# Kernel optimization log

Measured on AMD Instinct MI355X. Metric: run time of the kernel, lower is better.

## Reference

```python
import jax, jax.numpy as jnp
import numpy as np

NUM_HEADS = 4

def _pos_encoding(seq_len, d, dtype):
    # standard sinusoidal positional encoding [seq_len, d]
    pos = jnp.arange(seq_len, dtype=jnp.float32)[:, None]
    i = jnp.arange(0, d, 2, dtype=jnp.float32)
    div = jnp.exp(-jnp.log(10000.0) * i / d)
    ang = pos * div
    pe = jnp.zeros((seq_len, d), jnp.float32)
    pe = pe.at[:, 0::2].set(jnp.sin(ang)).at[:, 1::2].set(jnp.cos(ang))
    return pe.astype(dtype)

def _layer_norm(x, g, b, eps=1e-5):
    m = jnp.mean(x, axis=-1, keepdims=True)
    v = jnp.mean(jnp.square(x - m), axis=-1, keepdims=True)
    return (x - m) / jnp.sqrt(v + eps) * g + b

def setup_inputs() -> dict:
    key = jax.random.key(0)
    ks = jax.random.split(key, 10)
    B, S, H, W, N = 8, 512, 768, 8, 4096
    s = 0.02
    token_reps = jax.random.normal(ks[0], (B, S, H), jnp.float32)
    starts = jax.random.randint(ks[1], (B, N), 0, S - W)
    widths = jax.random.randint(ks[2], (B, N), 1, W + 1)
    span_ids = jnp.stack([starts, starts + widths], axis=-1)  # end > start, end <= S
    span_masks = jax.random.randint(ks[3], (B, N), 0, 2)
    return dict(
        token_reps=token_reps,
        dummy_query=jax.random.normal(ks[4], (H,), jnp.float32) * s,
        in_proj_w=jax.random.normal(ks[5], (3 * H, H), jnp.float32) * s,
        in_proj_b=jnp.zeros((3 * H,), jnp.float32),
        out_w=jax.random.normal(ks[6], (H, H), jnp.float32) * s,
        out_b=jnp.zeros((H,), jnp.float32),
        ln_g=jnp.ones((H,), jnp.float32),
        ln_b=jnp.zeros((H,), jnp.float32),
        ffn_w1=jax.random.normal(ks[7], (H, 4 * H), jnp.float32) * s,
        ffn_b1=jnp.zeros((4 * H,), jnp.float32),
        ffn_w2=jax.random.normal(ks[8], (4 * H, H), jnp.float32) * s,
        ffn_b2=jnp.zeros((H,), jnp.float32),
        span_ids=span_ids,
        span_masks=span_masks,
    )

def reference(token_reps, dummy_query, in_proj_w, in_proj_b, out_w, out_b,
              ln_g, ln_b, ffn_w1, ffn_b1, ffn_w2, ffn_b2, span_ids, span_masks):
    B, S, H = token_reps.shape
    N = span_ids.shape[1]
    NH = NUM_HEADS
    DH = H // NH
    # sequence positional encoding (dropout is identity in eval mode)
    x = token_reps + _pos_encoding(S, H, token_reps.dtype)[None]
    Wq, Wk, Wv = jnp.split(in_proj_w, 3, axis=0)
    bq, bk, bv = jnp.split(in_proj_b, 3)
    # single shared dummy query -> per-head query [NH, DH]
    q = (dummy_query @ Wq.T + bq).reshape(NH, DH)
    k = (x @ Wk.T + bk).reshape(B, S, NH, DH)
    v = (x @ Wv.T + bv).reshape(B, S, NH, DH)
    # scores are identical across spans since the query is shared: [B, NH, S]
    scores = jnp.einsum('hd,bshd->bhs', q, k) / jnp.sqrt(jnp.asarray(DH, x.dtype))
    pos = jnp.arange(S)
    # per-span key validity: start <= pos < end, and span not masked out  [B, N, S]
    valid = (pos[None, None, :] >= span_ids[..., 0:1]) & \
            (pos[None, None, :] < span_ids[..., 1:2]) & \
            (span_masks[..., None] != 0)
    logits = jnp.where(valid[:, :, None, :], scores[:, None, :, :], -1e9)  # [B,N,NH,S]
    w = jax.nn.softmax(logits, axis=-1)
    attn = jnp.einsum('bnhs,bshd->bnhd', w, v).reshape(B, N, H)
    attn = attn @ out_w.T + out_b
    h1 = _layer_norm(attn + dummy_query, ln_g, ln_b)
    ffn = jax.nn.relu(h1 @ ffn_w1 + ffn_b1) @ ffn_w2 + ffn_b2
    out = _layer_norm(ffn + h1, ln_g, ln_b)
    # masked spans produce exact zeros, matching the original loop
    return out * (span_masks[..., None] != 0).astype(out.dtype)
```

## Files before the change

kernel.cpp:

```cpp
#include <hip/hip_runtime.h>
#include <hip/hip_bf16.h>

#define Bb 8
#define Ss 512
#define Hh 768
#define NHh 4
#define Nn 4096
#define ROWS (Bb * Nn)
#define SCB 128

typedef _Float16 f16x8 __attribute__((ext_vector_type(8)));
typedef _Float16 f16x4 __attribute__((ext_vector_type(4)));
typedef _Float16 f16x2 __attribute__((ext_vector_type(2)));
typedef float f32x4 __attribute__((ext_vector_type(4)));

#define DEVINL __device__ __forceinline__

DEVINL void gld_lds16(const void* g, void* l) {
  __builtin_amdgcn_global_load_lds(
      (const __attribute__((address_space(1))) void*)g,
      (__attribute__((address_space(3))) void*)l, 16, 0, 0);
}

template <int V>
DEVINL void wait_vmcnt() {
  if constexpr (V == 0) asm volatile("s_waitcnt vmcnt(0)" ::: "memory");
  else if constexpr (V == 3) asm volatile("s_waitcnt vmcnt(3)" ::: "memory");
  else if constexpr (V == 4) asm volatile("s_waitcnt vmcnt(4)" ::: "memory");
  else if constexpr (V == 6) asm volatile("s_waitcnt vmcnt(6)" ::: "memory");
  else if constexpr (V == 8) asm volatile("s_waitcnt vmcnt(8)" ::: "memory");
}

DEVINL float block_sum256(float v, float* red) {
#pragma unroll
  for (int o = 32; o; o >>= 1) v += __shfl_xor(v, o, 64);
  const int wid = threadIdx.x >> 6, lane = threadIdx.x & 63;
  if (lane == 0) red[wid] = v;
  __syncthreads();
  float r = red[0] + red[1] + red[2] + red[3];
  __syncthreads();
  return r;
}

__global__ __launch_bounds__(256) void x_kernel(const float* __restrict__ tok,
                                                _Float16* __restrict__ x) {
  int idx = blockIdx.x * 256 + threadIdx.x;
  int t = idx % 384;
  int bs = idx / 384;
  int s = bs & (Ss - 1);
  float div = expf(-(float)t * 0.02398526138535465f);
  float ang = (float)s * div;
  float sv = sinf(ang), cv = cosf(ang);
  const float2 tv = ((const float2*)tok)[(size_t)bs * 384 + t];
  f16x2 o;
  o[0] = (_Float16)(tv.x + sv);
  o[1] = (_Float16)(tv.y + cv);
  *(f16x2*)&x[(size_t)bs * Hh + 2 * t] = o;
}

__global__ __launch_bounds__(256) void q_kernel(const float* __restrict__ dq,
                                                const float* __restrict__ ipw,
                                                const float* __restrict__ ipb,
                                                float* __restrict__ qout) {
  __shared__ float red[4];
  int o = blockIdx.x;
  const float* wr = ipw + (size_t)o * Hh;
  float s = 0.f;
#pragma unroll
  for (int e = 0; e < 3; e++) {
    int j = threadIdx.x + 256 * e;
    s += dq[j] * wr[j];
  }
  s = block_sum256(s, red);
  if (threadIdx.x == 0) qout[o] = s + ipb[o];
}

__global__ __launch_bounds__(256) void c_kernel(const float* __restrict__ q,
                                                const float* __restrict__ ipw,
                                                const float* __restrict__ ipb,
                                                float* __restrict__ cout,
                                                float* __restrict__ sbias) {
  __shared__ float red[4];
  int bid = blockIdx.x;
  int t = threadIdx.x;
  if (bid < 3072) {
    int h = bid / Hh;
    int j = bid - h * Hh;
    float s = 0.f;
    if (t < 192) s = q[h * 192 + t] * ipw[(size_t)(Hh + h * 192 + t) * Hh + j];
    s = block_sum256(s, red);
    if (t == 0) cout[bid] = s;
  } else {
    int h = bid - 3072;
    float s = 0.f;
    if (t < 192) s = q[h * 192 + t] * ipb[Hh + h * 192 + t];
    s = block_sum256(s, red);
    if (t == 0) sbias[h] = s;
  }
}

__global__ __launch_bounds__(256) void score_kernel(
    const _Float16* __restrict__ x, const float* __restrict__ c,
    const float* __restrict__ sbias, float* __restrict__ scores) {
  int bs = blockIdx.x;
  int wid = threadIdx.x >> 6, lane = threadIdx.x & 63;
  const _Float16* xr = x + (size_t)bs * Hh;
  const float* ch = c + wid * Hh;
  float s = 0.f;
#pragma unroll
  for (int e = 0; e < 12; e++) {
    int j = e * 64 + lane;
    s += (float)xr[j] * ch[j];
  }
#pragma unroll
  for (int o = 32; o; o >>= 1) s += __shfl_xor(s, o, 64);
  if (lane == 0) {
    int b = bs >> 9, pos = bs & (Ss - 1);
    scores[((size_t)(b * NHh + wid)) * Ss + pos] =
        (s + sbias[wid]) * 0.07216878364870322f;
  }
}

__global__ __launch_bounds__(256) void cvt_kernel(const float* __restrict__ in,
                                                  _Float16* __restrict__ out) {
  int i = blockIdx.x * 256 + threadIdx.x;
  float4 f = ((const float4*)in)[i];
  f16x4 o;
  o[0] = (_Float16)f.x;
  o[1] = (_Float16)f.y;
  o[2] = (_Float16)f.z;
  o[3] = (_Float16)f.w;
  ((f16x4*)out)[i] = o;
}

__global__ __launch_bounds__(256) void trcvt_kernel(const float* __restrict__ in,
                                                    _Float16* __restrict__ out,
                                                    int R, int C) {
  __shared__ float tile[32][33];
  int c0 = blockIdx.x * 32, r0 = blockIdx.y * 32;
  int tx = threadIdx.x & 31, ty0 = threadIdx.x >> 5;
#pragma unroll
  for (int ty = ty0; ty < 32; ty += 8)
    tile[ty][tx] = in[(size_t)(r0 + ty) * C + c0 + tx];
  __syncthreads();
#pragma unroll
  for (int ty = ty0; ty < 32; ty += 8)
    out[(size_t)(c0 + ty) * R + r0 + tx] = (_Float16)tile[tx][ty];
}

__global__ __launch_bounds__(256) void scan1_kernel(const int* __restrict__ mask,
                                                    int* __restrict__ bsum) {
  int r = blockIdx.x * 256 + threadIdx.x;
  unsigned long long b = __ballot(mask[r] != 0);
  __shared__ int wsum[4];
  int lane = threadIdx.x & 63, wid = threadIdx.x >> 6;
  if (lane == 0) wsum[wid] = __popcll(b);
  __syncthreads();
  if (threadIdx.x == 0)
    bsum[blockIdx.x] = wsum[0] + wsum[1] + wsum[2] + wsum[3];
}
__global__ __launch_bounds__(64) void scan2_kernel(const int* __restrict__ bsum,
                                                   int* __restrict__ boff,
                                                   int* __restrict__ cnt) {
  if (threadIdx.x == 0) {
    int acc = 0;
    for (int i = 0; i < SCB; i++) {
      boff[i] = acc;
      acc += bsum[i];
    }
    *cnt = acc;
  }
}
__global__ __launch_bounds__(256) void cidx_kernel(const int* __restrict__ mask,
                                                   const int* __restrict__ boff,
                                                   int* __restrict__ cidx) {
  int r = blockIdx.x * 256 + threadIdx.x;
  int m = mask[r] != 0;
  unsigned long long b = __ballot(m);
  __shared__ int wsum[4];
  int lane = threadIdx.x & 63, wid = threadIdx.x >> 6;
  if (lane == 0) wsum[wid] = __popcll(b);
  __syncthreads();
  int pre = 0;
#pragma unroll
  for (int i = 0; i < 3; i++)
    if (i < wid) pre += wsum[i];
  pre += __popcll(b & ((1ULL << lane) - 1));
  if (m) cidx[r] = boff[blockIdx.x] + pre;
}

template <int RELU, int BN>
__global__ __launch_bounds__(256, 2) void gemm_nt(
    const _Float16* __restrict__ A, const _Float16* __restrict__ W,
    const float* __restrict__ bias, _Float16* __restrict__ C, int N, int K,
    const int* __restrict__ mcount) {
  const long m0 = (long)blockIdx.x * 128;
  if (mcount && m0 >= (long)*mcount) return;
  __shared__ __align__(16) _Float16 As[3][128 * 32];
  __shared__ __align__(16) _Float16 Bs[3][BN * 32];
  const int tid = threadIdx.x;
  const int wid = tid >> 6;
  const int lane = tid & 63;
  const long n0 = (long)blockIdx.y * BN;
  constexpr int LPS = (BN == 128) ? 4 : 3;

  const int c0 = wid * 64 + lane;
  const int c1 = c0 + 256;
  const int sw0 = ((c0 & 3) ^ ((c0 >> 3) & 3)) * 8;
  const int sw1 = ((c1 & 3) ^ ((c1 >> 3) & 3)) * 8;
  const _Float16* gA0 = A + (m0 + (c0 >> 2)) * K + sw0;
  const _Float16* gA1 = A + (m0 + (c1 >> 2)) * K + sw1;
  const _Float16* gB0 = W + (n0 + (c0 >> 2)) * K + sw0;
  const _Float16* gB1 = W + (n0 + (c1 >> 2)) * K + sw1;

  const int wr = (wid >> 1) * 64;
  const int wc = (wid & 1) * (BN / 2);
  constexpr int NF = BN / 32;
  const int fr = lane & 15;
  const int fkb = lane >> 4;

  f32x4 acc[4][NF];
#pragma unroll
  for (int mi = 0; mi < 4; mi++)
#pragma unroll
    for (int ni = 0; ni < NF; ni++) acc[mi][ni] = (f32x4){0.f, 0.f, 0.f, 0.f};

#define STAGE(buf, k0)                                                  \
  do {                                                                  \
    gld_lds16(gA0 + (k0), &As[buf][wid * 512]);                         \
    gld_lds16(gA1 + (k0), &As[buf][2048 + wid * 512]);                  \
    gld_lds16(gB0 + (k0), &Bs[buf][wid * 512]);                         \
    if constexpr (BN == 128) gld_lds16(gB1 + (k0), &Bs[buf][2048 + wid * 512]); \
  } while (0)

#define COMPUTE(buf)                                                          \
  do {                                                                        \
    f16x8 af[4], bf[NF];                                                      \
    _Pragma("unroll") for (int i = 0; i < 4; i++) {                           \
      int r_ = wr + i * 16 + fr;                                              \
      af[i] = *(const f16x8*)&As[buf][r_ * 32 + ((fkb ^ ((r_ >> 1) & 3)) * 8)]; \
    }                                                                         \
    _Pragma("unroll") for (int i = 0; i < NF; i++) {                          \
      int r_ = wc + i * 16 + fr;                                              \
      bf[i] = *(const f16x8*)&Bs[buf][r_ * 32 + ((fkb ^ ((r_ >> 1) & 3)) * 8)]; \
    }                                                                         \
    _Pragma("unroll") for (int mi = 0; mi < 4; mi++)                          \
        _Pragma("unroll") for (int ni = 0; ni < NF; ni++)                     \
            acc[mi][ni] = __builtin_amdgcn_mfma_f32_16x16x32_f16(             \
                af[mi], bf[ni], acc[mi][ni], 0, 0, 0);                        \
  } while (0)

#define ITER_RESTAGE(b, knext)              \
  do {                                      \
    wait_vmcnt<2 * LPS>();                  \
    __builtin_amdgcn_s_barrier();           \
    COMPUTE(b);                             \
    __builtin_amdgcn_s_barrier();           \
    STAGE(b, (knext));                      \
  } while (0)

  const int nt = K >> 5;
  STAGE(0, 0);
  STAGE(1, 32);
  STAGE(2, 64);
  int t = 0;
  for (; t <= nt - 6; t += 3) {
    ITER_RESTAGE(0, (t + 3) * 32);
    ITER_RESTAGE(1, (t + 4) * 32);
    ITER_RESTAGE(2, (t + 5) * 32);
  }
  wait_vmcnt<2 * LPS>();
  __builtin_amdgcn_s_barrier();
  COMPUTE(0);
  wait_vmcnt<LPS>();
  __builtin_amdgcn_s_barrier();
  COMPUTE(1);
  wait_vmcnt<0>();
  __builtin_amdgcn_s_barrier();
  COMPUTE(2);
#undef STAGE
#undef COMPUTE
#undef ITER_RESTAGE

  const int crow = (lane >> 4) * 4;
  const int ccol = lane & 15;
  float bv[NF];
#pragma unroll
  for (int ni = 0; ni < NF; ni++)
    bv[ni] = bias ? bias[n0 + wc + ni * 16 + ccol] : 0.f;
#pragma unroll
  for (int mi = 0; mi < 4; mi++)
#pragma unroll
    for (int ni = 0; ni < NF; ni++)
#pragma unroll
      for (int i = 0; i < 4; i++) {
        float v = acc[mi][ni][i] + bv[ni];
        if (RELU) v = fmaxf(v, 0.f);
        C[(m0 + wr + mi * 16 + crow + i) * (long)N + (n0 + wc + ni * 16 + ccol)] =
            (_Float16)v;
      }
}

__global__ __launch_bounds__(256) void pool_kernel(
    const _Float16* __restrict__ v, const float* __restrict__ scores,
    const int* __restrict__ span_ids, const int* __restrict__ span_masks,
    _Float16* __restrict__ attn, const int* __restrict__ cidx) {
  int r = blockIdx.x;
  if (span_masks[r] == 0) return;
  int slot = cidx[r];
  int wid = threadIdx.x >> 6, lane = threadIdx.x & 63;
  _Float16* outr = attn + (size_t)slot * Hh;
  int b = r >> 12;
  int st = span_ids[2 * r], en = span_ids[2 * r + 1];
  int wdt = en - st;
  const float* sc = scores + ((size_t)(b * NHh + wid)) * Ss + st;
  float w[8];
  float mx = -1e30f;
#pragma unroll
  for (int j = 0; j < 8; j++) {
    float t = (j < wdt) ? sc[j] : -1e30f;
    w[j] = t;
    mx = fmaxf(mx, t);
  }
  float sum = 0.f;
#pragma unroll
  for (int j = 0; j < 8; j++) {
    float e = (j < wdt) ? expf(w[j] - mx) : 0.f;
    w[j] = e;
    sum += e;
  }
  float inv = 1.f / sum;
  float a0 = 0.f, a1 = 0.f, a2 = 0.f;
#pragma unroll
  for (int j = 0; j < 8; j++) {
    if (j < wdt) {
      const _Float16* vr =
          v + ((size_t)(b * Ss + st + j)) * Hh + wid * 192 + lane;
      float wj = w[j] * inv;
      a0 += wj * (float)vr[0];
      a1 += wj * (float)vr[64];
      a2 += wj * (float)vr[128];
    }
  }
  outr[wid * 192 + lane] = (_Float16)a0;
  outr[wid * 192 + 64 + lane] = (_Float16)a1;
  outr[wid * 192 + 128 + lane] = (_Float16)a2;
}

__global__ __launch_bounds__(256) void ln0_kernel(
    _Float16* __restrict__ X, const float* __restrict__ AddV,
    const float* __restrict__ g, const float* __restrict__ bta,
    const int* __restrict__ mcount) {
  __shared__ float red[4];
  int r = blockIdx.x;
  if (r >= *mcount) return;
  int t = threadIdx.x;
  float xv[3];
#pragma unroll
  for (int e = 0; e < 3; e++) {
    int d = t + 256 * e;
    xv[e] = (float)X[(size_t)r * Hh + d] + AddV[d];
  }
  float s = xv[0] + xv[1] + xv[2];
  s = block_sum256(s, red);
  float mean = s * (1.f / 768.f);
  float vs = 0.f;
#pragma unroll
  for (int e = 0; e < 3; e++) {
    float d = xv[e] - mean;
    vs += d * d;
  }
  vs = block_sum256(vs, red);
  float inv = rsqrtf(vs * (1.f / 768.f) + 1e-5f);
#pragma unroll
  for (int e = 0; e < 3; e++) {
    int d = t + 256 * e;
    X[(size_t)r * Hh + d] = (_Float16)((xv[e] - mean) * inv * g[d] + bta[d]);
  }
}

__global__ __launch_bounds__(256) void ln1_kernel(
    const _Float16* __restrict__ F2c, const _Float16* __restrict__ h1c,
    const int* __restrict__ cidx, const float* __restrict__ g,
    const float* __restrict__ bta, const int* __restrict__ mask,
    float* __restrict__ out) {
  __shared__ float red[4];
  int r = blockIdx.x;
  int t = threadIdx.x;
  float* orow = out + (size_t)r * Hh;
  if (mask[r] == 0) {
#pragma unroll
    for (int e = 0; e < 3; e++) orow[t + 256 * e] = 0.f;
    return;
  }
  int c = cidx[r];
  float xv[3];
#pragma unroll
  for (int e = 0; e < 3; e++) {
    int d = t + 256 * e;
    xv[e] = (float)F2c[(size_t)c * Hh + d] + (float)h1c[(size_t)c * Hh + d];
  }
  float s = xv[0] + xv[1] + xv[2];
  s = block_sum256(s, red);
  float mean = s * (1.f / 768.f);
  float vs = 0.f;
#pragma unroll
  for (int e = 0; e < 3; e++) {
    float d = xv[e] - mean;
    vs += d * d;
  }
  vs = block_sum256(vs, red);
  float inv = rsqrtf(vs * (1.f / 768.f) + 1e-5f);
#pragma unroll
  for (int e = 0; e < 3; e++) {
    int d = t + 256 * e;
    orow[d] = (xv[e] - mean) * inv * g[d] + bta[d];
  }
}

extern "C" void kernel_launch(void* const* d_in, const int* in_sizes, int n_in,
                              void* d_out, int out_size, void* d_ws,
                              size_t ws_size, hipStream_t stream) {
  (void)out_size;
  if (n_in != 14) return;
  if (in_sizes[0] != 3145728 || in_sizes[2] != 1769472 ||
      in_sizes[3] != 2304 || in_sizes[4] != 589824 ||
      in_sizes[8] != 2359296 || in_sizes[9] != 3072 ||
      in_sizes[12] != 65536 || in_sizes[13] != 32768)
    return;

  const float* tok   = (const float*)d_in[0];
  const float* dq    = (const float*)d_in[1];
  const float* ipw   = (const float*)d_in[2];
  const float* ipb   = (const float*)d_in[3];
  const float* outw  = (const float*)d_in[4];
  const float* outb  = (const float*)d_in[5];
  const float* lng   = (const float*)d_in[6];
  const float* lnb   = (const float*)d_in[7];
  const float* w1    = (const float*)d_in[8];
  const float* b1    = (const float*)d_in[9];
  const float* w2    = (const float*)d_in[10];
  const float* b2    = (const float*)d_in[11];
  const int* spid    = (const int*)d_in[12];
  const int* spmask  = (const int*)d_in[13];

  char* ws = (char*)d_ws;
  size_t off = 0;
  auto alloc = [&](size_t bytes) {
    size_t r = off;
    off = (off + bytes + 255) & ~(size_t)255;
    return r;
  };
  _Float16* X16  = (_Float16*)(ws + alloc((size_t)Bb * Ss * Hh * 2));
  float* SC      = (float*)(ws + alloc((size_t)Bb * NHh * Ss * 4));
  float* Q       = (float*)(ws + alloc(768 * 4));
  float* Cc      = (float*)(ws + alloc(3072 * 4));
  float* SB      = (float*)(ws + alloc(4 * 4));
  _Float16* WV16 = (_Float16*)(ws + alloc((size_t)768 * 768 * 2));
  _Float16* OW16 = (_Float16*)(ws + alloc((size_t)768 * 768 * 2));
  _Float16* WT1  = (_Float16*)(ws + alloc((size_t)3072 * 768 * 2));
  _Float16* WT2  = (_Float16*)(ws + alloc((size_t)768 * 3072 * 2));
  _Float16* ATTN = (_Float16*)(ws + alloc((size_t)ROWS * Hh * 2));
  _Float16* PROJ = (_Float16*)(ws + alloc((size_t)ROWS * Hh * 2));
  _Float16* F1   = (_Float16*)(ws + alloc((size_t)ROWS * 3072 * 2));
  if (ws_size < off) return;
  _Float16* F2 = ATTN;

  int* CIDX = (int*)X16;
  int* BSUM = (int*)X16 + ROWS;
  int* BOFF = (int*)X16 + ROWS + SCB;
  int* CNT  = (int*)X16 + ROWS + 2 * SCB;

  _Float16* V16 = (_Float16*)d_out;

  cvt_kernel<<<576, 256, 0, stream>>>(ipw + (size_t)1536 * 768, WV16);
  cvt_kernel<<<576, 256, 0, stream>>>(outw, OW16);
  trcvt_kernel<<<dim3(96, 24), 256, 0, stream>>>(w1, WT1, 768, 3072);
  trcvt_kernel<<<dim3(24, 96), 256, 0, stream>>>(w2, WT2, 3072, 768);

  x_kernel<<<(Bb * Ss * 384) / 256, 256, 0, stream>>>(tok, X16);
  q_kernel<<<768, 256, 0, stream>>>(dq, ipw, ipb, Q);
  c_kernel<<<3076, 256, 0, stream>>>(Q, ipw, ipb, Cc, SB);
  score_kernel<<<Bb * Ss, 256, 0, stream>>>(X16, Cc, SB, SC);
  gemm_nt<0, 64><<<dim3(32, 12), 256, 0, stream>>>(X16, WV16, ipb + 1536, V16,
                                                   768, 768, nullptr);
  scan1_kernel<<<SCB, 256, 0, stream>>>(spmask, BSUM);
  scan2_kernel<<<1, 64, 0, stream>>>(BSUM, BOFF, CNT);
  cidx_kernel<<<SCB, 256, 0, stream>>>(spmask, BOFF, CIDX);
  pool_kernel<<<ROWS, 256, 0, stream>>>(V16, SC, spid, spmask, ATTN, CIDX);
  gemm_nt<0, 128><<<dim3(ROWS / 128, 6), 256, 0, stream>>>(ATTN, OW16, outb,
                                                           PROJ, 768, 768, CNT);
  ln0_kernel<<<ROWS, 256, 0, stream>>>(PROJ, dq, lng, lnb, CNT);
  gemm_nt<1, 128><<<dim3(ROWS / 128, 24), 256, 0, stream>>>(PROJ, WT1, b1, F1,
                                                            3072, 768, CNT);
  gemm_nt<0, 128><<<dim3(ROWS / 128, 6), 256, 0, stream>>>(F1, WT2, b2, F2,
                                                           768, 3072, CNT);
  ln1_kernel<<<ROWS, 256, 0, stream>>>(F2, PROJ, CIDX, lng, lnb, spmask,
                                       (float*)d_out);
}
```

Before: 403.8 us.

## Group GEMM tiles by 8 M-blocks, raise MFMA priority, vectorize pooling

The GEMMs move from a 2D grid to a 1D grid that is remapped so that groups of 8 consecutive M tiles sweep every N tile. This is meant to improve L2 reuse of the A rows, and with the early exit on the compacted row count, skipped blocks become contiguous groups. MFMA sections are wrapped with s_setprio so waves in the compute phase get scheduling priority over loads. The pooling kernel now uses 192 threads that each handle 4 contiguous halfs with vector loads and stores, instead of 256 threads doing strided scalar accesses.

```diff
diff --git a/kernel.cpp b/kernel.cpp
--- a/kernel.cpp
+++ b/kernel.cpp
@@ -193,15 +193,18 @@
 __global__ __launch_bounds__(256, 2) void gemm_nt(
     const _Float16* __restrict__ A, const _Float16* __restrict__ W,
     const float* __restrict__ bias, _Float16* __restrict__ C, int N, int K,
-    const int* __restrict__ mcount) {
-  const long m0 = (long)blockIdx.x * 128;
+    int nn, const int* __restrict__ mcount) {
+  const int bid = (int)blockIdx.x;
+  const int mi = (bid >> 3) / nn;
+  const int nt_ = (bid >> 3) - mi * nn;
+  const long m0 = (long)(mi * 8 + (bid & 7)) * 128;
+  const long n0 = (long)nt_ * BN;
   if (mcount && m0 >= (long)*mcount) return;
   __shared__ __align__(16) _Float16 As[3][128 * 32];
   __shared__ __align__(16) _Float16 Bs[3][BN * 32];
   const int tid = threadIdx.x;
   const int wid = tid >> 6;
   const int lane = tid & 63;
-  const long n0 = (long)blockIdx.y * BN;
   constexpr int LPS = (BN == 128) ? 4 : 3;
 
   const int c0 = wid * 64 + lane;
@@ -221,9 +224,9 @@
 
   f32x4 acc[4][NF];
 #pragma unroll
-  for (int mi = 0; mi < 4; mi++)
-#pragma unroll
-    for (int ni = 0; ni < NF; ni++) acc[mi][ni] = (f32x4){0.f, 0.f, 0.f, 0.f};
+  for (int mi2 = 0; mi2 < 4; mi2++)
+#pragma unroll
+    for (int ni = 0; ni < NF; ni++) acc[mi2][ni] = (f32x4){0.f, 0.f, 0.f, 0.f};
 
 #define STAGE(buf, k0)                                                  \
   do {                                                                  \
@@ -244,10 +247,12 @@
       int r_ = wc + i * 16 + fr;                                              \
       bf[i] = *(const f16x8*)&Bs[buf][r_ * 32 + ((fkb ^ ((r_ >> 1) & 3)) * 8)]; \
     }                                                                         \
-    _Pragma("unroll") for (int mi = 0; mi < 4; mi++)                          \
+    __builtin_amdgcn_s_setprio(1);                                            \
+    _Pragma("unroll") for (int mi2 = 0; mi2 < 4; mi2++)                       \
         _Pragma("unroll") for (int ni = 0; ni < NF; ni++)                     \
-            acc[mi][ni] = __builtin_amdgcn_mfma_f32_16x16x32_f16(             \
-                af[mi], bf[ni], acc[mi][ni], 0, 0, 0);                        \
+            acc[mi2][ni] = __builtin_amdgcn_mfma_f32_16x16x32_f16(            \
+                af[mi2], bf[ni], acc[mi2][ni], 0, 0, 0);                      \
+    __builtin_amdgcn_s_setprio(0);                                            \
   } while (0)
 
 #define ITER_RESTAGE(b, knext)              \
@@ -289,31 +294,32 @@
   for (int ni = 0; ni < NF; ni++)
     bv[ni] = bias ? bias[n0 + wc + ni * 16 + ccol] : 0.f;
 #pragma unroll
-  for (int mi = 0; mi < 4; mi++)
+  for (int mi2 = 0; mi2 < 4; mi2++)
 #pragma unroll
     for (int ni = 0; ni < NF; ni++)
 #pragma unroll
       for (int i = 0; i < 4; i++) {
-        float v = acc[mi][ni][i] + bv[ni];
+        float v = acc[mi2][ni][i] + bv[ni];
         if (RELU) v = fmaxf(v, 0.f);
-        C[(m0 + wr + mi * 16 + crow + i) * (long)N + (n0 + wc + ni * 16 + ccol)] =
+        C[(m0 + wr + mi2 * 16 + crow + i) * (long)N + (n0 + wc + ni * 16 + ccol)] =
             (_Float16)v;
       }
 }
 
-__global__ __launch_bounds__(256) void pool_kernel(
+__global__ __launch_bounds__(192) void pool_kernel(
     const _Float16* __restrict__ v, const float* __restrict__ scores,
     const int* __restrict__ span_ids, const int* __restrict__ span_masks,
     _Float16* __restrict__ attn, const int* __restrict__ cidx) {
   int r = blockIdx.x;
   if (span_masks[r] == 0) return;
   int slot = cidx[r];
-  int wid = threadIdx.x >> 6, lane = threadIdx.x & 63;
-  _Float16* outr = attn + (size_t)slot * Hh;
+  int i = threadIdx.x;
+  int h = i / 48;
+  int d0 = i * 4;
   int b = r >> 12;
   int st = span_ids[2 * r], en = span_ids[2 * r + 1];
   int wdt = en - st;
-  const float* sc = scores + ((size_t)(b * NHh + wid)) * Ss + st;
+  const float* sc = scores + ((size_t)(b * NHh + h)) * Ss + st;
   float w[8];
   float mx = -1e30f;
 #pragma unroll
@@ -330,21 +336,24 @@
     sum += e;
   }
   float inv = 1.f / sum;
-  float a0 = 0.f, a1 = 0.f, a2 = 0.f;
+  float a0 = 0.f, a1 = 0.f, a2 = 0.f, a3 = 0.f;
 #pragma unroll
   for (int j = 0; j < 8; j++) {
     if (j < wdt) {
-      const _Float16* vr =
-          v + ((size_t)(b * Ss + st + j)) * Hh + wid * 192 + lane;
+      f16x4 vv = *(const f16x4*)(v + ((size_t)(b * Ss + st + j)) * Hh + d0);
       float wj = w[j] * inv;
-      a0 += wj * (float)vr[0];
-      a1 += wj * (float)vr[64];
-      a2 += wj * (float)vr[128];
+      a0 += wj * (float)vv[0];
+      a1 += wj * (float)vv[1];
+      a2 += wj * (float)vv[2];
+      a3 += wj * (float)vv[3];
     }
   }
-  outr[wid * 192 + lane] = (_Float16)a0;
-  outr[wid * 192 + 64 + lane] = (_Float16)a1;
-  outr[wid * 192 + 128 + lane] = (_Float16)a2;
+  f16x4 o;
+  o[0] = (_Float16)a0;
+  o[1] = (_Float16)a1;
+  o[2] = (_Float16)a2;
+  o[3] = (_Float16)a3;
+  *(f16x4*)&attn[(size_t)slot * Hh + d0] = o;
 }
 
 __global__ __launch_bounds__(256) void ln0_kernel(
@@ -482,19 +491,19 @@
   q_kernel<<<768, 256, 0, stream>>>(dq, ipw, ipb, Q);
   c_kernel<<<3076, 256, 0, stream>>>(Q, ipw, ipb, Cc, SB);
   score_kernel<<<Bb * Ss, 256, 0, stream>>>(X16, Cc, SB, SC);
-  gemm_nt<0, 64><<<dim3(32, 12), 256, 0, stream>>>(X16, WV16, ipb + 1536, V16,
-                                                   768, 768, nullptr);
+  gemm_nt<0, 64><<<384, 256, 0, stream>>>(X16, WV16, ipb + 1536, V16,
+                                          768, 768, 12, nullptr);
   scan1_kernel<<<SCB, 256, 0, stream>>>(spmask, BSUM);
   scan2_kernel<<<1, 64, 0, stream>>>(BSUM, BOFF, CNT);
   cidx_kernel<<<SCB, 256, 0, stream>>>(spmask, BOFF, CIDX);
-  pool_kernel<<<ROWS, 256, 0, stream>>>(V16, SC, spid, spmask, ATTN, CIDX);
-  gemm_nt<0, 128><<<dim3(ROWS / 128, 6), 256, 0, stream>>>(ATTN, OW16, outb,
-                                                           PROJ, 768, 768, CNT);
+  pool_kernel<<<ROWS, 192, 0, stream>>>(V16, SC, spid, spmask, ATTN, CIDX);
+  gemm_nt<0, 128><<<1536, 256, 0, stream>>>(ATTN, OW16, outb, PROJ,
+                                            768, 768, 6, CNT);
   ln0_kernel<<<ROWS, 256, 0, stream>>>(PROJ, dq, lng, lnb, CNT);
-  gemm_nt<1, 128><<<dim3(ROWS / 128, 24), 256, 0, stream>>>(PROJ, WT1, b1, F1,
-                                                            3072, 768, CNT);
-  gemm_nt<0, 128><<<dim3(ROWS / 128, 6), 256, 0, stream>>>(F1, WT2, b2, F2,
-                                                           768, 3072, CNT);
+  gemm_nt<1, 128><<<6144, 256, 0, stream>>>(PROJ, WT1, b1, F1,
+                                            3072, 768, 24, CNT);
+  gemm_nt<0, 128><<<1536, 256, 0, stream>>>(F1, WT2, b2, F2,
+                                            768, 3072, 6, CNT);
   ln1_kernel<<<ROWS, 256, 0, stream>>>(F2, PROJ, CIDX, lng, lnb, spmask,
                                        (float*)d_out);
 }
```

Measured after the change: 413.5 us. 1.02x slower.
